# Kernel tuning notes

Measured on AMD Instinct MI355X. Metric: run time of the kernel, lower is better.

The kernel has to match this reference:

```python
import jax, jax.numpy as jnp
import numpy as np

B, S, D, F = 4, 4096, 1024, 256


def _ln(x, g, b, eps=1e-5):
    m = x.mean(-1, keepdims=True)
    v = ((x - m) ** 2).mean(-1, keepdims=True)
    return (x - m) / jnp.sqrt(v + eps) * g + b


def setup_inputs() -> dict:
    key = jax.random.key(0)
    ks = jax.random.split(key, 8)
    return {
        "x": jax.random.normal(ks[0], (B, S, D), jnp.float32),
        "W_to": jax.random.normal(ks[1], (2 * F, D), jnp.float32) * 0.02,   # to_spectral.weight [out,in]
        "log_decay": jnp.zeros((F,), jnp.float32),
        "frequencies": jax.random.normal(ks[2], (F,), jnp.float32) * 0.01,
        "W_from": jax.random.normal(ks[3], (D, 2 * F), jnp.float32) * 0.02,  # from_spectral.weight
        "ln1_g": jnp.ones((D,), jnp.float32), "ln1_b": jnp.zeros((D,), jnp.float32),
        "ln3_g": jnp.ones((D,), jnp.float32), "ln3_b": jnp.zeros((D,), jnp.float32),
        "W_ffn1": jax.random.normal(ks[4], (4 * D, D), jnp.float32) * 0.02,
        "b_ffn1": jnp.zeros((4 * D,), jnp.float32),
        "W_ffn2": jax.random.normal(ks[5], (D, 4 * D), jnp.float32) * 0.02,
        "b_ffn2": jnp.zeros((D,), jnp.float32),
    }


def reference(x, W_to, log_decay, frequencies, W_from, ln1_g, ln1_b,
              ln3_g, ln3_b, W_ffn1, b_ffn1, W_ffn2, b_ffn2):
    Bc, Sc, Dc = x.shape
    Fc = log_decay.shape[0]
    dt = 1.0  # registered buffer dt = 1.0

    residual = x
    h = _ln(x, ln1_g, ln1_b)
    spec = jnp.einsum('bsd,fd->bsf', h, W_to)          # [B,S,2F]
    real, imag = spec[..., :Fc], spec[..., Fc:]

    decay = jax.nn.sigmoid(log_decay)                   # [F]
    omega = jnp.tanh(frequencies) * 0.1
    c, s = jnp.cos(omega * dt), jnp.sin(omega * dt)

    def step(carry, u):
        sr, si = carry
        r, i = u                                        # [B,F]
        sr = sr * decay + r * 0.1
        si = si * decay + i * 0.1
        nr = jnp.clip(sr * c - si * s, -10.0, 10.0)
        ni = jnp.clip(sr * s + si * c, -10.0, 10.0)
        return (nr, ni), (nr, ni)

    init = (jnp.zeros((Bc, Fc), x.dtype), jnp.zeros((Bc, Fc), x.dtype))
    _, (out_r, out_i) = jax.lax.scan(
        step, init, (real.transpose(1, 0, 2), imag.transpose(1, 0, 2)))
    spectral_out = jnp.concatenate(
        [out_r.transpose(1, 0, 2), out_i.transpose(1, 0, 2)], axis=-1)  # [B,S,2F]

    h = jnp.einsum('bsf,df->bsd', spectral_out, W_from)
    x2 = residual + h * 0.1

    # FFN block (dropout = identity in eval)
    r3 = x2
    h = _ln(x2, ln3_g, ln3_b)
    h = jnp.einsum('bsd,ed->bse', h, W_ffn1) + b_ffn1
    h = jax.nn.gelu(h, approximate=False)               # nn.GELU default = exact erf
    h = jnp.einsum('bse,de->bsd', h, W_ffn2) + b_ffn2
    return r3 + h * 0.1
```

## Files before the change

kernel.cpp:

```cpp
#include <hip/hip_runtime.h>
#include <hip/hip_bf16.h>
#include <math.h>

typedef _Float16 f16x8 __attribute__((ext_vector_type(8)));
typedef _Float16 f16x4 __attribute__((ext_vector_type(4)));
typedef float f32x4 __attribute__((ext_vector_type(4)));
typedef float f32x16 __attribute__((ext_vector_type(16)));
typedef int v4i __attribute__((ext_vector_type(4)));
typedef int v8i __attribute__((ext_vector_type(8)));

#define GAS __attribute__((address_space(1)))
#define LAS __attribute__((address_space(3)))

__device__ __forceinline__ void async_load16(const void* g, void* l) {
  __builtin_amdgcn_global_load_lds((const GAS void*)g, (LAS void*)l, 16, 0, 0);
}

__device__ __forceinline__ float fast_gelu(float x) {
  float x3 = x * x * x;
  float u = 0.7978845608f * x + 0.0356774081f * x3;
  float e = __expf(2.0f * u);
  float t = 1.0f - 2.0f / (e + 1.0f);
  return 0.5f * x * (1.0f + t);
}

__device__ __forceinline__ int pack4_fp8(float a, float b, float c, float d) {
  int p = __builtin_amdgcn_cvt_pk_fp8_f32(a, b, 0, false);
  p = __builtin_amdgcn_cvt_pk_fp8_f32(c, d, p, true);
  return p;
}

__global__ __launch_bounds__(256) void cvt_all_kernel(
    const float* __restrict__ W_to, const float* __restrict__ W_from,
    const float* __restrict__ W_ffn1, const float* __restrict__ W_ffn2,
    _Float16* __restrict__ Wto_h, _Float16* __restrict__ Wfrom_h,
    unsigned char* __restrict__ Wf1_8, unsigned char* __restrict__ Wf2_8) {
  int id = blockIdx.x * 256 + threadIdx.x;
  if (id < 131072) {
    int i = id * 4;
    float4 v = *(const float4*)(W_to + i);
    f16x4 o;
    o.x = (_Float16)v.x; o.y = (_Float16)v.y; o.z = (_Float16)v.z; o.w = (_Float16)v.w;
    *(f16x4*)(Wto_h + i) = o;
  } else if (id < 262144) {
    int i = (id - 131072) * 4;
    float4 v = *(const float4*)(W_from + i);
    f16x4 o;
    o.x = (_Float16)v.x; o.y = (_Float16)v.y; o.z = (_Float16)v.z; o.w = (_Float16)v.w;
    *(f16x4*)(Wfrom_h + i) = o;
  } else if (id < 1310720) {
    int i = (id - 262144) * 4;
    float4 v = *(const float4*)(W_ffn1 + i);
    *(int*)(Wf1_8 + i) = pack4_fp8(v.x, v.y, v.z, v.w);
  } else {
    int id2 = id - 1310720;
    int n = id2 >> 10;
    int p0 = (id2 & 1023) * 4;
    int p7 = p0 & 127;
    int grp = (p7 >> 2) & 3;
    int h = (p7 >> 4) & 1;
    int k_src = (p0 & ~127) | (p7 & 96) | (grp << 3) | (h << 2);
    float4 v = *(const float4*)(W_ffn2 + (size_t)n * 4096 + k_src);
    *(int*)(Wf2_8 + (size_t)n * 4096 + p0) = pack4_fp8(v.x, v.y, v.z, v.w);
  }
}

template <int OUT8>
__global__ __launch_bounds__(256) void ln_kernel(const float* __restrict__ x,
                                                 const float* __restrict__ gamma,
                                                 const float* __restrict__ beta,
                                                 _Float16* __restrict__ outH,
                                                 unsigned char* __restrict__ outB) {
  int row = blockIdx.x;
  int t = threadIdx.x;
  float4 v = ((const float4*)(x + (size_t)row * 1024))[t];
  float s = v.x + v.y + v.z + v.w;
  float s2 = v.x * v.x + v.y * v.y + v.z * v.z + v.w * v.w;
#pragma unroll
  for (int o = 32; o > 0; o >>= 1) { s += __shfl_xor(s, o); s2 += __shfl_xor(s2, o); }
  __shared__ float red[8];
  int w = t >> 6;
  if ((t & 63) == 0) { red[w] = s; red[4 + w] = s2; }
  __syncthreads();
  s = red[0] + red[1] + red[2] + red[3];
  s2 = red[4] + red[5] + red[6] + red[7];
  float mean = s * (1.0f / 1024.0f);
  float var = s2 * (1.0f / 1024.0f) - mean * mean;
  float rstd = rsqrtf(var + 1e-5f);
  float4 gv = ((const float4*)gamma)[t];
  float4 bv = ((const float4*)beta)[t];
  float y0 = (v.x - mean) * rstd * gv.x + bv.x;
  float y1 = (v.y - mean) * rstd * gv.y + bv.y;
  float y2 = (v.z - mean) * rstd * gv.z + bv.z;
  float y3 = (v.w - mean) * rstd * gv.w + bv.w;
  if (OUT8) {
    *(int*)(outB + (size_t)row * 1024 + t * 4) = pack4_fp8(y0, y1, y2, y3);
  } else {
    f16x4 o;
    o.x = (_Float16)y0; o.y = (_Float16)y1; o.z = (_Float16)y2; o.w = (_Float16)y3;
    *(f16x4*)(outH + (size_t)row * 1024 + t * 4) = o;
  }
}

#define SCAN_CH 64
#define SCAN_W 64
__global__ __launch_bounds__(256) void scan_kernel(const _Float16* __restrict__ spec,
                                                   const float* __restrict__ log_decay,
                                                   const float* __restrict__ freq,
                                                   _Float16* __restrict__ so) {
  const int S = 4096;
  const int nchunks = S / SCAN_CH;
  int f = threadIdx.x;
  int b = blockIdx.x / nchunks;
  int ck = blockIdx.x % nchunks;
  int t0 = ck * SCAN_CH;
  int ts = (ck == 0) ? 0 : (t0 - SCAN_W);
  int nsteps = t0 + SCAN_CH - ts;

  float decay = 1.0f / (1.0f + expf(-log_decay[f]));
  float om = tanhf(freq[f]) * 0.1f;
  float co = cosf(om);
  float sn = sinf(om);
  float sr = 0.0f, si = 0.0f;

  const _Float16* base = spec + (size_t)b * S * 512;
  _Float16* ob = so + (size_t)b * S * 512;

  float rb[8], ib[8];
#pragma unroll
  for (int j = 0; j < 8; j++) {
    rb[j] = (float)base[(size_t)(ts + j) * 512 + f];
    ib[j] = (float)base[(size_t)(ts + j) * 512 + 256 + f];
  }
  for (int gs = 0; gs < nsteps; gs += 8) {
    float cr[8], ci[8];
#pragma unroll
    for (int j = 0; j < 8; j++) { cr[j] = rb[j]; ci[j] = ib[j]; }
    if (gs + 8 < nsteps) {
      int nx = ts + gs + 8;
#pragma unroll
      for (int j = 0; j < 8; j++) {
        rb[j] = (float)base[(size_t)(nx + j) * 512 + f];
        ib[j] = (float)base[(size_t)(nx + j) * 512 + 256 + f];
      }
    }
#pragma unroll
    for (int j = 0; j < 8; j++) {
      int t = ts + gs + j;
      sr = sr * decay + cr[j] * 0.1f;
      si = si * decay + ci[j] * 0.1f;
      float nr = sr * co - si * sn;
      float ni = sr * sn + si * co;
      nr = fminf(10.0f, fmaxf(-10.0f, nr));
      ni = fminf(10.0f, fmaxf(-10.0f, ni));
      sr = nr; si = ni;
      if (t >= t0) {
        ob[(size_t)t * 512 + f] = (_Float16)nr;
        ob[(size_t)t * 512 + 256 + f] = (_Float16)ni;
      }
    }
  }
}

template <int EPI>
__global__ __launch_bounds__(256, 2) void gemm_nt_kernel(
    const _Float16* __restrict__ A, const _Float16* __restrict__ Bm,
    const float* __restrict__ bias, const float* resid,
    float* outF, _Float16* __restrict__ outH,
    int M, int N, int K, int lda, int ldb) {
  __shared__ __align__(16) _Float16 As[2][128 * 32];
  __shared__ __align__(16) _Float16 Bs[2][128 * 32];
  const int tid = threadIdx.x;
  const int lane = tid & 63;
  const int wave = tid >> 6;
  const int wm = (wave >> 1) * 64;
  const int wn = (wave & 1) * 64;
  const int bm = blockIdx.x * 128;
  const int bn = blockIdx.y * 128;

  size_t ga[2], gb[2];
  int lo[2];
#pragma unroll
  for (int rep = 0; rep < 2; rep++) {
    int lsi = tid + rep * 256;
    int row = lsi >> 2;
    int slot = lsi & 3;
    int sw = (row ^ (row >> 2)) & 3;
    int gseg = slot ^ sw;
    lo[rep] = lsi * 8;
    ga[rep] = (size_t)(bm + row) * lda + (size_t)gseg * 8;
    gb[rep] = (size_t)(bn + row) * ldb + (size_t)gseg * 8;
  }

  const int q = lane >> 4;
  const int ml = lane & 15;
  int aaddr[4], baddr[4];
#pragma unroll
  for (int i = 0; i < 4; i++) {
    int r = wm + i * 16 + ml;
    aaddr[i] = (r * 4 + (q ^ ((r ^ (r >> 2)) & 3))) * 8;
    int rn = wn + i * 16 + ml;
    baddr[i] = (rn * 4 + (q ^ ((rn ^ (rn >> 2)) & 3))) * 8;
  }

  const f32x4 zero = {0.0f, 0.0f, 0.0f, 0.0f};
  f32x4 acc[4][4];
#pragma unroll
  for (int i = 0; i < 4; i++)
#pragma unroll
    for (int j = 0; j < 4; j++) acc[i][j] = zero;

  for (int k0 = 0; k0 < K; k0 += 64) {
    __syncthreads();
#pragma unroll
    for (int h = 0; h < 2; h++) {
#pragma unroll
      for (int rep = 0; rep < 2; rep++) {
        async_load16(A + ga[rep] + k0 + h * 32, &As[h][lo[rep]]);
        async_load16(Bm + gb[rep] + k0 + h * 32, &Bs[h][lo[rep]]);
      }
    }
    __syncthreads();
#pragma unroll
    for (int h = 0; h < 2; h++) {
      f16x8 af[4], bf[4];
#pragma unroll
      for (int i = 0; i < 4; i++) {
        af[i] = *(const f16x8*)(As[h] + aaddr[i]);
        bf[i] = *(const f16x8*)(Bs[h] + baddr[i]);
      }
#pragma unroll
      for (int i = 0; i < 4; i++)
#pragma unroll
        for (int j = 0; j < 4; j++)
          acc[i][j] = __builtin_amdgcn_mfma_f32_16x16x32_f16(bf[j], af[i], acc[i][j], 0, 0, 0);
    }
  }

#pragma unroll
  for (int i = 0; i < 4; i++) {
    int gm = bm + wm + i * 16 + ml;
#pragma unroll
    for (int j = 0; j < 4; j++) {
      int gn = bn + wn + j * 16 + q * 4;
      size_t idx = (size_t)gm * N + gn;
      f32x4 c = acc[i][j];
      if (EPI == 0) {
        f16x4 o;
        o.x = (_Float16)c[0]; o.y = (_Float16)c[1];
        o.z = (_Float16)c[2]; o.w = (_Float16)c[3];
        *(f16x4*)(outH + idx) = o;
      } else {
        float4 rv = *(const float4*)(resid + idx);
        float4 bv = bias ? *(const float4*)(bias + gn) : float4{0.f, 0.f, 0.f, 0.f};
        float4 o;
        o.x = rv.x + 0.1f * (c[0] + bv.x);
        o.y = rv.y + 0.1f * (c[1] + bv.y);
        o.z = rv.z + 0.1f * (c[2] + bv.z);
        o.w = rv.w + 0.1f * (c[3] + bv.w);
        *(float4*)(outF + idx) = o;
      }
    }
  }
}

template <int EPI>
__global__ __launch_bounds__(256, 3) void gemm_fp8_kernel(
    const unsigned char* __restrict__ A, const unsigned char* __restrict__ Bm,
    const float* __restrict__ bias, const float* resid,
    float* outF, unsigned char* __restrict__ outB,
    int M, int N, int K, int lda, int ldb) {
  __shared__ __align__(16) unsigned char As[2][128 * 64];
  __shared__ __align__(16) unsigned char Bs[2][128 * 64];
  const int tid = threadIdx.x;
  const int lane = tid & 63;
  const int wave = tid >> 6;
  const int wm = (wave >> 1) * 64;
  const int wn = (wave & 1) * 64;
  const int bm = blockIdx.x * 128;
  const int bn = blockIdx.y * 128;

  size_t ga[2], gb[2];
  int lo[2];
#pragma unroll
  for (int rep = 0; rep < 2; rep++) {
    int lsi = tid + rep * 256;
    int row = lsi >> 2;
    int slot = lsi & 3;
    int sw = (row ^ (row >> 2)) & 3;
    int gseg = slot ^ sw;
    lo[rep] = lsi * 16;
    ga[rep] = (size_t)(bm + row) * lda + (size_t)gseg * 16;
    gb[rep] = (size_t)(bn + row) * ldb + (size_t)gseg * 16;
  }

  const int ml = lane & 31;
  const int h2 = lane >> 5;
  int aaddr[2][2], baddr[2][2];
#pragma unroll
  for (int t = 0; t < 2; t++) {
    int r = wm + t * 32 + ml;
    int sw = (r ^ (r >> 2)) & 3;
    aaddr[t][0] = (r * 4 + ((2 * h2) ^ sw)) * 16;
    aaddr[t][1] = (r * 4 + ((2 * h2 + 1) ^ sw)) * 16;
    int rn = wn + t * 32 + ml;
    int swn = (rn ^ (rn >> 2)) & 3;
    baddr[t][0] = (rn * 4 + ((2 * h2) ^ swn)) * 16;
    baddr[t][1] = (rn * 4 + ((2 * h2 + 1) ^ swn)) * 16;
  }

  f32x16 acc[2][2];
#pragma unroll
  for (int i = 0; i < 2; i++)
#pragma unroll
    for (int j = 0; j < 2; j++)
#pragma unroll
      for (int r = 0; r < 16; r++) acc[i][j][r] = 0.0f;

  for (int k0 = 0; k0 < K; k0 += 128) {
    __syncthreads();
#pragma unroll
    for (int h = 0; h < 2; h++) {
#pragma unroll
      for (int rep = 0; rep < 2; rep++) {
        async_load16(A + ga[rep] + k0 + h * 64, &As[h][lo[rep]]);
        async_load16(Bm + gb[rep] + k0 + h * 64, &Bs[h][lo[rep]]);
      }
    }
    __syncthreads();
#pragma unroll
    for (int h = 0; h < 2; h++) {
      const unsigned char* Ab = As[h];
      const unsigned char* Bb = Bs[h];
      v8i af[2], bf[2];
#pragma unroll
      for (int tt = 0; tt < 2; tt++) {
        v4i a0 = *(const v4i*)(Ab + aaddr[tt][0]);
        v4i a1 = *(const v4i*)(Ab + aaddr[tt][1]);
        af[tt] = __builtin_shufflevector(a0, a1, 0, 1, 2, 3, 4, 5, 6, 7);
        v4i b0 = *(const v4i*)(Bb + baddr[tt][0]);
        v4i b1 = *(const v4i*)(Bb + baddr[tt][1]);
        bf[tt] = __builtin_shufflevector(b0, b1, 0, 1, 2, 3, 4, 5, 6, 7);
      }
#pragma unroll
      for (int i = 0; i < 2; i++)
#pragma unroll
        for (int j = 0; j < 2; j++)
          acc[i][j] = __builtin_amdgcn_mfma_scale_f32_32x32x64_f8f6f4(
              bf[j], af[i], acc[i][j], 0, 0, 0, 0x7F7F7F7F, 0, 0x7F7F7F7F);
    }
  }

#pragma unroll
  for (int i = 0; i < 2; i++) {
    int gm = bm + wm + i * 32 + ml;
#pragma unroll
    for (int j = 0; j < 2; j++) {
      if (EPI == 2) {
        int w[4];
#pragma unroll
        for (int grp = 0; grp < 4; grp++) {
          int n0 = bn + wn + j * 32 + grp * 8 + h2 * 4;
          float4 bv = *(const float4*)(bias + n0);
          float v0 = fast_gelu(acc[i][j][grp * 4 + 0] + bv.x);
          float v1 = fast_gelu(acc[i][j][grp * 4 + 1] + bv.y);
          float v2 = fast_gelu(acc[i][j][grp * 4 + 2] + bv.z);
          float v3 = fast_gelu(acc[i][j][grp * 4 + 3] + bv.w);
          w[grp] = pack4_fp8(v0, v1, v2, v3);
        }
        int pbase = bn + wn + j * 32 + h2 * 16;
        v4i pk = {w[0], w[1], w[2], w[3]};
        *(v4i*)(outB + (size_t)gm * N + pbase) = pk;
      } else {
#pragma unroll
        for (int grp = 0; grp < 4; grp++) {
          int n0 = bn + wn + j * 32 + grp * 8 + h2 * 4;
          size_t idx = (size_t)gm * N + n0;
          float4 rv = *(const float4*)(resid + idx);
          float4 bv = *(const float4*)(bias + n0);
          float4 o;
          o.x = rv.x + 0.1f * (acc[i][j][grp * 4 + 0] + bv.x);
          o.y = rv.y + 0.1f * (acc[i][j][grp * 4 + 1] + bv.y);
          o.z = rv.z + 0.1f * (acc[i][j][grp * 4 + 2] + bv.z);
          o.w = rv.w + 0.1f * (acc[i][j][grp * 4 + 3] + bv.w);
          *(float4*)(outF + idx) = o;
        }
      }
    }
  }
}

extern "C" void kernel_launch(void* const* d_in, const int* in_sizes, int n_in,
                              void* d_out, int out_size, void* d_ws, size_t ws_size,
                              hipStream_t stream) {
  const int Bb = 4, S = 4096, D = 1024, F = 256;
  const int M = Bb * S;
  const int N1 = 2 * F;
  const int NF = 4 * D;

  const float* x       = (const float*)d_in[0];
  const float* W_to    = (const float*)d_in[1];
  const float* log_dec = (const float*)d_in[2];
  const float* freq    = (const float*)d_in[3];
  const float* W_from  = (const float*)d_in[4];
  const float* ln1_g   = (const float*)d_in[5];
  const float* ln1_b   = (const float*)d_in[6];
  const float* ln3_g   = (const float*)d_in[7];
  const float* ln3_b   = (const float*)d_in[8];
  const float* W_ffn1  = (const float*)d_in[9];
  const float* b_ffn1  = (const float*)d_in[10];
  const float* W_ffn2  = (const float*)d_in[11];
  const float* b_ffn2  = (const float*)d_in[12];
  float* out = (float*)d_out;
  (void)in_sizes; (void)n_in; (void)out_size; (void)ws_size;

  char* ws = (char*)d_ws;
  _Float16*      Wto_h   = (_Float16*)(ws);
  _Float16*      Wfrom_h = (_Float16*)(ws + (size_t)1048576);
  unsigned char* Wf1_8   = (unsigned char*)(ws + (size_t)2097152);
  unsigned char* Wf2_8   = (unsigned char*)(ws + (size_t)6291456);
  char* dyn = ws + (size_t)10485760;
  _Float16*      h16     = (_Float16*)(dyn);
  _Float16*      so      = (_Float16*)(dyn);
  _Float16*      spec16  = (_Float16*)(dyn + (size_t)33554432);
  unsigned char* h8      = (unsigned char*)(dyn + (size_t)50331648);
  unsigned char* g8      = (unsigned char*)(dyn + (size_t)67108864);

  cvt_all_kernel<<<9216, 256, 0, stream>>>(W_to, W_from, W_ffn1, W_ffn2,
                                           Wto_h, Wfrom_h, Wf1_8, Wf2_8);

  ln_kernel<0><<<M, 256, 0, stream>>>(x, ln1_g, ln1_b, h16, nullptr);

  gemm_nt_kernel<0><<<dim3(M / 128, N1 / 128), 256, 0, stream>>>(
      h16, Wto_h, nullptr, nullptr, nullptr, spec16, M, N1, D, D, D);

  scan_kernel<<<Bb * (S / SCAN_CH), 256, 0, stream>>>(spec16, log_dec, freq, so);

  gemm_nt_kernel<1><<<dim3(M / 128, D / 128), 256, 0, stream>>>(
      so, Wfrom_h, nullptr, x, out, nullptr, M, D, N1, N1, N1);

  ln_kernel<1><<<M, 256, 0, stream>>>(out, ln3_g, ln3_b, nullptr, h8);

  gemm_fp8_kernel<2><<<dim3(M / 128, NF / 128), 256, 0, stream>>>(
      h8, Wf1_8, b_ffn1, nullptr, nullptr, g8, M, NF, D, D, D);

  gemm_fp8_kernel<1><<<dim3(M / 128, D / 128), 256, 0, stream>>>(
      g8, Wf2_8, b_ffn2, out, out, nullptr, M, D, NF, NF, NF);
}
```

Baseline: 471.6 us.

## Rewrite FP8 FFN GEMMs with 256x256 tiles and 4-stage async pipeline

Replaces the 128x128 double-buffered FP8 GEMMs for both FFN layers with 256x256-tile kernels using 512 threads, a 4-deep LDS ring, partial vmcnt waits and s_setprio around the MFMA blocks. This raises reuse per loaded byte and hides global-load latency. It also halves the scan warm-up window and raises the occupancy hint on the fp16 GEMM. The large tiles need 128KB of LDS and fewer blocks; the shorter scan warm-up may change accuracy.

```diff
diff --git a/kernel.cpp b/kernel.cpp
--- a/kernel.cpp
+++ b/kernel.cpp
@@ -103,7 +103,7 @@
 }
 
 #define SCAN_CH 64
-#define SCAN_W 64
+#define SCAN_W 32
 __global__ __launch_bounds__(256) void scan_kernel(const _Float16* __restrict__ spec,
                                                    const float* __restrict__ log_decay,
                                                    const float* __restrict__ freq,
@@ -163,7 +163,7 @@
 }
 
 template <int EPI>
-__global__ __launch_bounds__(256, 2) void gemm_nt_kernel(
+__global__ __launch_bounds__(256, 3) void gemm_nt_kernel(
     const _Float16* __restrict__ A, const _Float16* __restrict__ Bm,
     const float* __restrict__ bias, const float* resid,
     float* outF, _Float16* __restrict__ outH,
@@ -264,131 +264,179 @@
   }
 }
 
-template <int EPI>
-__global__ __launch_bounds__(256, 3) void gemm_fp8_kernel(
+
+#define FP8_256_PROLOG                                                        \
+  __shared__ __align__(16) unsigned char As[4][256 * 64];                     \
+  __shared__ __align__(16) unsigned char Bs[4][256 * 64];                     \
+  const int tid = threadIdx.x;                                                \
+  const int lane = tid & 63;                                                  \
+  const int wave = tid >> 6;                                                  \
+  const int wm = (wave >> 2) * 128;                                           \
+  const int wn = (wave & 3) * 64;                                             \
+  const int bm = blockIdx.x * 256;                                            \
+  const int bn = blockIdx.y * 256;                                            \
+  size_t ga[2], gb[2];                                                        \
+  int lo[2];                                                                  \
+  _Pragma("unroll")                                                           \
+  for (int rep = 0; rep < 2; rep++) {                                         \
+    int lsi = tid + rep * 512;                                                \
+    int row = lsi >> 2;                                                       \
+    int slot = lsi & 3;                                                       \
+    int sw = (row ^ (row >> 2)) & 3;                                          \
+    int gseg = slot ^ sw;                                                     \
+    lo[rep] = lsi * 16;                                                       \
+    ga[rep] = (size_t)(bm + row) * lda + (size_t)gseg * 16;                   \
+    gb[rep] = (size_t)(bn + row) * ldb + (size_t)gseg * 16;                   \
+  }                                                                           \
+  const int ml = lane & 31;                                                   \
+  const int h2 = lane >> 5;                                                   \
+  int aaddr[4][2], baddr[2][2];                                               \
+  _Pragma("unroll")                                                           \
+  for (int i = 0; i < 4; i++) {                                               \
+    int r = wm + i * 32 + ml;                                                 \
+    int sw = (r ^ (r >> 2)) & 3;                                              \
+    aaddr[i][0] = (r * 4 + ((2 * h2) ^ sw)) * 16;                             \
+    aaddr[i][1] = (r * 4 + ((2 * h2 + 1) ^ sw)) * 16;                         \
+  }                                                                           \
+  _Pragma("unroll")                                                           \
+  for (int j = 0; j < 2; j++) {                                               \
+    int rn = wn + j * 32 + ml;                                                \
+    int sw = (rn ^ (rn >> 2)) & 3;                                            \
+    baddr[j][0] = (rn * 4 + ((2 * h2) ^ sw)) * 16;                            \
+    baddr[j][1] = (rn * 4 + ((2 * h2 + 1) ^ sw)) * 16;                        \
+  }                                                                           \
+  f32x16 acc[4][2];                                                           \
+  _Pragma("unroll")                                                           \
+  for (int i = 0; i < 4; i++)                                                 \
+    _Pragma("unroll")                                                         \
+    for (int j = 0; j < 2; j++)                                               \
+      _Pragma("unroll")                                                       \
+      for (int r = 0; r < 16; r++) acc[i][j][r] = 0.0f;                       \
+  const int NT = K >> 6;
+
+#define STAGE_T(s, t)                                                         \
+  {                                                                           \
+    _Pragma("unroll")                                                         \
+    for (int rep = 0; rep < 2; rep++) {                                       \
+      async_load16(A + ga[rep] + (size_t)(t) * 64, &As[s][lo[rep]]);          \
+      async_load16(Bm + gb[rep] + (size_t)(t) * 64, &Bs[s][lo[rep]]);         \
+    }                                                                         \
+  }
+
+#define COMPUTE_T(s)                                                          \
+  {                                                                           \
+    v8i bf[2];                                                                \
+    _Pragma("unroll")                                                         \
+    for (int j = 0; j < 2; j++) {                                             \
+      v4i* bp = (v4i*)&bf[j];                                                 \
+      bp[0] = *(const v4i*)(Bs[s] + baddr[j][0]);                             \
+      bp[1] = *(const v4i*)(Bs[s] + baddr[j][1]);                             \
+    }                                                                         \
+    __builtin_amdgcn_s_setprio(1);                                            \
+    _Pragma("unroll")                                                         \
+    for (int i = 0; i < 4; i++) {                                             \
+      v8i af;                                                                 \
+      v4i* ap = (v4i*)&af;                                                    \
+      ap[0] = *(const v4i*)(As[s] + aaddr[i][0]);                             \
+      ap[1] = *(const v4i*)(As[s] + aaddr[i][1]);                             \
+      acc[i][0] = __builtin_amdgcn_mfma_scale_f32_32x32x64_f8f6f4(            \
+          bf[0], af, acc[i][0], 0, 0, 0, 0x7F7F7F7F, 0, 0x7F7F7F7F);          \
+      acc[i][1] = __builtin_amdgcn_mfma_scale_f32_32x32x64_f8f6f4(            \
+          bf[1], af, acc[i][1], 0, 0, 0, 0x7F7F7F7F, 0, 0x7F7F7F7F);          \
+    }                                                                         \
+    __builtin_amdgcn_s_setprio(0);                                            \
+  }
+
+#define SYNC_T(vmc)                                                           \
+  asm volatile("s_waitcnt vmcnt(" #vmc ") lgkmcnt(0)" ::: "memory");          \
+  __builtin_amdgcn_s_barrier();
+
+#define FP8_256_MAIN_LOOP                                                     \
+  STAGE_T(0, 0)                                                               \
+  STAGE_T(1, 1)                                                               \
+  STAGE_T(2, 2)                                                               \
+  SYNC_T(8)                                                                   \
+  for (int t4 = 0; t4 + 8 <= NT; t4 += 4) {                                   \
+    _Pragma("unroll")                                                         \
+    for (int u = 0; u < 4; u++) {                                             \
+      STAGE_T((u + 3) & 3, t4 + u + 3)                                        \
+      COMPUTE_T(u)                                                            \
+      SYNC_T(8)                                                               \
+    }                                                                         \
+  }                                                                           \
+  STAGE_T(3, NT - 1)                                                          \
+  COMPUTE_T(0)                                                                \
+  SYNC_T(8)                                                                   \
+  COMPUTE_T(1)                                                                \
+  SYNC_T(4)                                                                   \
+  COMPUTE_T(2)                                                                \
+  SYNC_T(0)                                                                   \
+  COMPUTE_T(3)
+
+__global__ __launch_bounds__(512, 1) void gemm3_fp8_256(
     const unsigned char* __restrict__ A, const unsigned char* __restrict__ Bm,
-    const float* __restrict__ bias, const float* resid,
-    float* outF, unsigned char* __restrict__ outB,
+    const float* __restrict__ bias, unsigned char* __restrict__ outB,
     int M, int N, int K, int lda, int ldb) {
-  __shared__ __align__(16) unsigned char As[2][128 * 64];
-  __shared__ __align__(16) unsigned char Bs[2][128 * 64];
-  const int tid = threadIdx.x;
-  const int lane = tid & 63;
-  const int wave = tid >> 6;
-  const int wm = (wave >> 1) * 64;
-  const int wn = (wave & 1) * 64;
-  const int bm = blockIdx.x * 128;
-  const int bn = blockIdx.y * 128;
-
-  size_t ga[2], gb[2];
-  int lo[2];
-#pragma unroll
-  for (int rep = 0; rep < 2; rep++) {
-    int lsi = tid + rep * 256;
-    int row = lsi >> 2;
-    int slot = lsi & 3;
-    int sw = (row ^ (row >> 2)) & 3;
-    int gseg = slot ^ sw;
-    lo[rep] = lsi * 16;
-    ga[rep] = (size_t)(bm + row) * lda + (size_t)gseg * 16;
-    gb[rep] = (size_t)(bn + row) * ldb + (size_t)gseg * 16;
-  }
-
-  const int ml = lane & 31;
-  const int h2 = lane >> 5;
-  int aaddr[2][2], baddr[2][2];
-#pragma unroll
-  for (int t = 0; t < 2; t++) {
-    int r = wm + t * 32 + ml;
-    int sw = (r ^ (r >> 2)) & 3;
-    aaddr[t][0] = (r * 4 + ((2 * h2) ^ sw)) * 16;
-    aaddr[t][1] = (r * 4 + ((2 * h2 + 1) ^ sw)) * 16;
-    int rn = wn + t * 32 + ml;
-    int swn = (rn ^ (rn >> 2)) & 3;
-    baddr[t][0] = (rn * 4 + ((2 * h2) ^ swn)) * 16;
-    baddr[t][1] = (rn * 4 + ((2 * h2 + 1) ^ swn)) * 16;
-  }
-
-  f32x16 acc[2][2];
-#pragma unroll
-  for (int i = 0; i < 2; i++)
-#pragma unroll
-    for (int j = 0; j < 2; j++)
-#pragma unroll
-      for (int r = 0; r < 16; r++) acc[i][j][r] = 0.0f;
-
-  for (int k0 = 0; k0 < K; k0 += 128) {
-    __syncthreads();
-#pragma unroll
-    for (int h = 0; h < 2; h++) {
-#pragma unroll
-      for (int rep = 0; rep < 2; rep++) {
-        async_load16(A + ga[rep] + k0 + h * 64, &As[h][lo[rep]]);
-        async_load16(Bm + gb[rep] + k0 + h * 64, &Bs[h][lo[rep]]);
-      }
-    }
-    __syncthreads();
-#pragma unroll
-    for (int h = 0; h < 2; h++) {
-      const unsigned char* Ab = As[h];
-      const unsigned char* Bb = Bs[h];
-      v8i af[2], bf[2];
-#pragma unroll
-      for (int tt = 0; tt < 2; tt++) {
-        v4i a0 = *(const v4i*)(Ab + aaddr[tt][0]);
-        v4i a1 = *(const v4i*)(Ab + aaddr[tt][1]);
-        af[tt] = __builtin_shufflevector(a0, a1, 0, 1, 2, 3, 4, 5, 6, 7);
-        v4i b0 = *(const v4i*)(Bb + baddr[tt][0]);
-        v4i b1 = *(const v4i*)(Bb + baddr[tt][1]);
-        bf[tt] = __builtin_shufflevector(b0, b1, 0, 1, 2, 3, 4, 5, 6, 7);
-      }
-#pragma unroll
-      for (int i = 0; i < 2; i++)
-#pragma unroll
-        for (int j = 0; j < 2; j++)
-          acc[i][j] = __builtin_amdgcn_mfma_scale_f32_32x32x64_f8f6f4(
-              bf[j], af[i], acc[i][j], 0, 0, 0, 0x7F7F7F7F, 0, 0x7F7F7F7F);
-    }
-  }
-
-#pragma unroll
-  for (int i = 0; i < 2; i++) {
+  FP8_256_PROLOG
+  FP8_256_MAIN_LOOP
+
+#pragma unroll
+  for (int i = 0; i < 4; i++) {
     int gm = bm + wm + i * 32 + ml;
 #pragma unroll
     for (int j = 0; j < 2; j++) {
-      if (EPI == 2) {
-        int w[4];
-#pragma unroll
-        for (int grp = 0; grp < 4; grp++) {
-          int n0 = bn + wn + j * 32 + grp * 8 + h2 * 4;
-          float4 bv = *(const float4*)(bias + n0);
-          float v0 = fast_gelu(acc[i][j][grp * 4 + 0] + bv.x);
-          float v1 = fast_gelu(acc[i][j][grp * 4 + 1] + bv.y);
-          float v2 = fast_gelu(acc[i][j][grp * 4 + 2] + bv.z);
-          float v3 = fast_gelu(acc[i][j][grp * 4 + 3] + bv.w);
-          w[grp] = pack4_fp8(v0, v1, v2, v3);
-        }
-        int pbase = bn + wn + j * 32 + h2 * 16;
-        v4i pk = {w[0], w[1], w[2], w[3]};
-        *(v4i*)(outB + (size_t)gm * N + pbase) = pk;
-      } else {
-#pragma unroll
-        for (int grp = 0; grp < 4; grp++) {
-          int n0 = bn + wn + j * 32 + grp * 8 + h2 * 4;
-          size_t idx = (size_t)gm * N + n0;
-          float4 rv = *(const float4*)(resid + idx);
-          float4 bv = *(const float4*)(bias + n0);
-          float4 o;
-          o.x = rv.x + 0.1f * (acc[i][j][grp * 4 + 0] + bv.x);
-          o.y = rv.y + 0.1f * (acc[i][j][grp * 4 + 1] + bv.y);
-          o.z = rv.z + 0.1f * (acc[i][j][grp * 4 + 2] + bv.z);
-          o.w = rv.w + 0.1f * (acc[i][j][grp * 4 + 3] + bv.w);
-          *(float4*)(outF + idx) = o;
-        }
-      }
-    }
-  }
-}
+      int w[4];
+#pragma unroll
+      for (int grp = 0; grp < 4; grp++) {
+        int n0 = bn + wn + j * 32 + grp * 8 + h2 * 4;
+        float4 bv = *(const float4*)(bias + n0);
+        float v0 = fast_gelu(acc[i][j][grp * 4 + 0] + bv.x);
+        float v1 = fast_gelu(acc[i][j][grp * 4 + 1] + bv.y);
+        float v2 = fast_gelu(acc[i][j][grp * 4 + 2] + bv.z);
+        float v3 = fast_gelu(acc[i][j][grp * 4 + 3] + bv.w);
+        w[grp] = pack4_fp8(v0, v1, v2, v3);
+      }
+      int pbase = bn + wn + j * 32 + h2 * 16;
+      v4i pk = {w[0], w[1], w[2], w[3]};
+      *(v4i*)(outB + (size_t)gm * N + pbase) = pk;
+    }
+  }
+}
+
+__global__ __launch_bounds__(512, 1) void gemm4_fp8_256(
+    const unsigned char* __restrict__ A, const unsigned char* __restrict__ Bm,
+    const float* __restrict__ bias, const float* resid, float* outF,
+    int M, int N, int K, int lda, int ldb) {
+  FP8_256_PROLOG
+  FP8_256_MAIN_LOOP
+
+#pragma unroll
+  for (int i = 0; i < 4; i++) {
+    int gm = bm + wm + i * 32 + ml;
+#pragma unroll
+    for (int j = 0; j < 2; j++) {
+#pragma unroll
+      for (int grp = 0; grp < 4; grp++) {
+        int n0 = bn + wn + j * 32 + grp * 8 + h2 * 4;
+        size_t idx = (size_t)gm * N + n0;
+        float4 rv = *(const float4*)(resid + idx);
+        float4 bv = *(const float4*)(bias + n0);
+        float4 o;
+        o.x = rv.x + 0.1f * (acc[i][j][grp * 4 + 0] + bv.x);
+        o.y = rv.y + 0.1f * (acc[i][j][grp * 4 + 1] + bv.y);
+        o.z = rv.z + 0.1f * (acc[i][j][grp * 4 + 2] + bv.z);
+        o.w = rv.w + 0.1f * (acc[i][j][grp * 4 + 3] + bv.w);
+        *(float4*)(outF + idx) = o;
+      }
+    }
+  }
+}
+
+#undef STAGE_T
+#undef COMPUTE_T
+#undef SYNC_T
+#undef FP8_256_PROLOG
+#undef FP8_256_MAIN_LOOP
 
 extern "C" void kernel_launch(void* const* d_in, const int* in_sizes, int n_in,
                               void* d_out, int out_size, void* d_ws, size_t ws_size,
@@ -441,9 +489,9 @@
 
   ln_kernel<1><<<M, 256, 0, stream>>>(out, ln3_g, ln3_b, nullptr, h8);
 
-  gemm_fp8_kernel<2><<<dim3(M / 128, NF / 128), 256, 0, stream>>>(
-      h8, Wf1_8, b_ffn1, nullptr, nullptr, g8, M, NF, D, D, D);
-
-  gemm_fp8_kernel<1><<<dim3(M / 128, D / 128), 256, 0, stream>>>(
-      g8, Wf2_8, b_ffn2, out, out, nullptr, M, D, NF, NF, NF);
-}
+  gemm3_fp8_256<<<dim3(M / 256, NF / 256), 512, 0, stream>>>(
+      h8, Wf1_8, b_ffn1, g8, M, NF, D, D, D);
+
+  gemm4_fp8_256<<<dim3(M / 256, D / 256), 512, 0, stream>>>(
+      g8, Wf2_8, b_ffn2, out, out, M, D, NF, NF, NF);
+}
```

Result: slower. 500.4 us (+6.1%).
